# Optimization experiments

Hardware: AMD Instinct MI355X
Metric: run time of the kernel (lower is better)

## Reference

```python
import jax, jax.numpy as jnp
import numpy as np

B, T, U, D = 2, 512, 48, 512
H, K = 1024, 128  # hidden_channels, num_classes; fc1 in = 2*D = 1024


def setup_inputs() -> dict:
    key = jax.random.key(0)
    ks = jax.random.split(key, 9)
    s = 0.02
    return {
        "img_feature": jax.random.normal(ks[0], (B, T, D), jnp.float32),
        "label_feature": jax.random.normal(ks[1], (B, U, D), jnp.float32),
        "masks": jnp.ones((B, 1, T), jnp.float32),
        "W1": jax.random.normal(ks[2], (H, 2 * D), jnp.float32) * s,
        "b1": jnp.zeros((H,), jnp.float32),
        "W2": jax.random.normal(ks[3], (K, H), jnp.float32) * s,
        "b2": jnp.zeros((K,), jnp.float32),
        "conv_w": jax.random.normal(ks[4], (K, D), jnp.float32) * s,
        "conv_b": jnp.zeros((K,), jnp.float32),
    }


def reference(img_feature, label_feature, masks, W1, b1, W2, b2, conv_w, conv_b):
    # pointwise Conv1d over img features: (B,T,D) -> (B,K,T), masked
    img_seg_score = (jnp.einsum('btd,kd->bkt', img_feature, conv_w)
                     + conv_b[None, :, None]) * masks
    # fc1(cat(label, img)) == label @ Wl^T + img @ Wi^T + b1 (broadcast add),
    # avoiding the O(B*U*T*2D) repeat+cat intermediate.
    d = label_feature.shape[-1]
    Wl, Wi = W1[:, :d], W1[:, d:]
    lab = jnp.einsum('bud,hd->buh', label_feature, Wl)  # (B,U,H)
    img = jnp.einsum('btd,hd->bth', img_feature, Wi)    # (B,T,H)
    h = jnp.tanh(lab[:, :, None, :] + img[:, None, :, :] + b1)  # (B,U,T,H)
    joint = jnp.einsum('buth,kh->butk', h, W2) + b2
    joint_score = jax.nn.log_softmax(joint, axis=-1)
    return (img_seg_score, joint_score)
```

## Files before the change

kernel.cpp:

```cpp
#include <hip/hip_runtime.h>
#include <math.h>

#define BB 2
#define TT 512
#define UU 48
#define DD 512
#define HH 1024
#define KK 128

typedef _Float16 f16x8 __attribute__((ext_vector_type(8)));
typedef __fp16 fp16x2_t __attribute__((ext_vector_type(2)));
typedef float floatx4 __attribute__((ext_vector_type(4)));

__device__ __forceinline__ void g2l16(const _Float16* g, _Float16* l) {
    __builtin_amdgcn_global_load_lds(
        (const __attribute__((address_space(1))) unsigned int*)g,
        (__attribute__((address_space(3))) unsigned int*)l, 16, 0, 0);
}

__device__ __forceinline__ f16x8 tanh8(f16x8 x) {
    f16x8 o;
#pragma unroll
    for (int i = 0; i < 8; i += 2) {
        float s0 = (float)x[i];
        float s1 = (float)x[i + 1];
        float e0 = __expf(s0 + s0);
        float e1 = __expf(s1 + s1);
        float r0 = __builtin_amdgcn_rcpf(e0 + 1.0f);
        float r1 = __builtin_amdgcn_rcpf(e1 + 1.0f);
        fp16x2_t p = __builtin_amdgcn_cvt_pkrtz(fmaf(-2.0f, r0, 1.0f),
                                                fmaf(-2.0f, r1, 1.0f));
        o[i] = (_Float16)p[0];
        o[i + 1] = (_Float16)p[1];
    }
    return o;
}

__global__ __launch_bounds__(256) void mid_kernel4(
    const float* __restrict__ img, const float* __restrict__ labf,
    const float* __restrict__ W1, const float* __restrict__ W2,
    const float* __restrict__ conv_w,
    const float* __restrict__ b1, const float* __restrict__ conv_b,
    const float* __restrict__ masks,
    _Float16* __restrict__ imgHf, _Float16* __restrict__ labHf,
    _Float16* __restrict__ W2s, float* __restrict__ seg_out) {
    int bid = blockIdx.x, tid = threadIdx.x;
    if (bid >= 312) {
        int base = (bid - 312) * 256 + tid;
#pragma unroll
        for (int i = 0; i < 32; ++i) {
            int o = base + i * 4096;
            int hg = o >> 10, kk2 = (o >> 3) & 127, hl = o & 7;
            W2s[o] = (_Float16)W2[(size_t)kk2 * HH + hg * 8 + hl];
        }
        return;
    }
    __shared__ __align__(16) _Float16 a_s[32][72];
    __shared__ __align__(16) _Float16 w_s[8192];
    const float* Arow;
    const float* Wbase;
    int r0, n0b, wstride, region;
    if (bid < 256) {
        region = 0; Arow = img; Wbase = W1 + 512; wstride = 1024;
        r0 = (bid & 31) * 32; n0b = (bid >> 5) * 128;
    } else if (bid < 280) {
        region = 1; Arow = labf; Wbase = W1; wstride = 1024;
        int i = bid - 256; r0 = (i % 3) * 32; n0b = (i / 3) * 128;
    } else {
        region = 2; Arow = img; Wbase = conv_w; wstride = 512;
        r0 = (bid - 280) * 32; n0b = 0;
    }
    int lane = tid & 63, wv = tid >> 6;
    int m0 = (wv & 1) * 16, n0w = (wv >> 1) * 64;
    int q = lane >> 4, r = lane & 15;
    int arow = tid >> 3, acol = (tid & 7) * 8;
    int wn = tid >> 3, wk = tid & 7;
    const float* aptr = &Arow[(size_t)(r0 + arow) * DD + acol];
    floatx4 acc[4] = {};
    float4 pa0, pa1, pw[4][2];
    pa0 = *(const float4*)aptr;
    pa1 = *(const float4*)(aptr + 4);
#pragma unroll
    for (int i2 = 0; i2 < 4; ++i2) {
        const float* wp_ = &Wbase[(size_t)(n0b + i2 * 32 + wn) * wstride + wk * 8];
        pw[i2][0] = *(const float4*)wp_;
        pw[i2][1] = *(const float4*)(wp_ + 4);
    }
    for (int c = 0; c < 8; ++c) {
        {
            f16x8 av;
            av[0] = (_Float16)pa0.x; av[1] = (_Float16)pa0.y;
            av[2] = (_Float16)pa0.z; av[3] = (_Float16)pa0.w;
            av[4] = (_Float16)pa1.x; av[5] = (_Float16)pa1.y;
            av[6] = (_Float16)pa1.z; av[7] = (_Float16)pa1.w;
            *(f16x8*)&a_s[arow][acol] = av;
#pragma unroll
            for (int i2 = 0; i2 < 4; ++i2) {
                f16x8 wvv;
                wvv[0] = (_Float16)pw[i2][0].x; wvv[1] = (_Float16)pw[i2][0].y;
                wvv[2] = (_Float16)pw[i2][0].z; wvv[3] = (_Float16)pw[i2][0].w;
                wvv[4] = (_Float16)pw[i2][1].x; wvv[5] = (_Float16)pw[i2][1].y;
                wvv[6] = (_Float16)pw[i2][1].z; wvv[7] = (_Float16)pw[i2][1].w;
                *(f16x8*)&w_s[((size_t)wk * 128 + i2 * 32 + wn) * 8] = wvv;
            }
        }
        __syncthreads();
        if (c < 7) {
            int cb = (c + 1) * 64;
            pa0 = *(const float4*)(aptr + cb);
            pa1 = *(const float4*)(aptr + cb + 4);
#pragma unroll
            for (int i2 = 0; i2 < 4; ++i2) {
                const float* wp_ =
                    &Wbase[(size_t)(n0b + i2 * 32 + wn) * wstride + cb + wk * 8];
                pw[i2][0] = *(const float4*)wp_;
                pw[i2][1] = *(const float4*)(wp_ + 4);
            }
        }
#pragma unroll
        for (int kt = 0; kt < 2; ++kt) {
            f16x8 af = *(const f16x8*)&a_s[m0 + r][kt * 32 + q * 8];
#pragma unroll
            for (int nt = 0; nt < 4; ++nt) {
                f16x8 bfv = *(const f16x8*)
                    &w_s[((kt * 4 + q) * 128 + n0w + nt * 16 + r) * 8];
                acc[nt] = __builtin_amdgcn_mfma_f32_16x16x32_f16(
                    af, bfv, acc[nt], 0, 0, 0);
            }
        }
        __syncthreads();
    }
    if (region == 0) {
#pragma unroll
        for (int nt = 0; nt < 4; ++nt) {
            int n = n0b + n0w + nt * 16 + r;
#pragma unroll
            for (int rr = 0; rr < 4; ++rr)
                imgHf[(size_t)(r0 + m0 + 4 * q + rr) * HH + n] =
                    (_Float16)acc[nt][rr];
        }
    } else if (region == 1) {
#pragma unroll
        for (int nt = 0; nt < 4; ++nt) {
            int n = n0b + n0w + nt * 16 + r;
            float bv = b1[n];
#pragma unroll
            for (int rr = 0; rr < 4; ++rr)
                labHf[(size_t)(r0 + m0 + 4 * q + rr) * HH + n] =
                    (_Float16)(acc[nt][rr] + bv);
        }
    } else {
#pragma unroll
        for (int nt = 0; nt < 4; ++nt) {
            int k = n0w + nt * 16 + r;
            float bv = conv_b[k];
#pragma unroll
            for (int rr = 0; rr < 4; ++rr) {
                int row = r0 + m0 + 4 * q + rr;
                int b = row >> 9, t = row & 511;
                seg_out[((size_t)b * KK + k) * TT + t] =
                    (acc[nt][rr] + bv) * masks[row];
            }
        }
    }
}

__global__ __launch_bounds__(256) void joint_kernel8(
    const _Float16* __restrict__ imgHf,
    const _Float16* __restrict__ labHf,
    const _Float16* __restrict__ W2s,
    const float* __restrict__ b2,
    float* __restrict__ out) {
    __shared__ __align__(16) _Float16 w_s[2][8192];
    int tid = threadIdx.x, bid = blockIdx.x;
    int t0 = (bid & 7) * 64;
    int rest = bid >> 3;
    int u = rest % UU, b = rest / UU;
    int lane = tid & 63, wv = tid >> 6;
    int q = lane >> 4, r = lane & 15;
    const _Float16* imgrow = imgHf + ((size_t)b * TT + t0 + wv * 16 + r) * HH;
    const _Float16* labrow = labHf + (size_t)(b * UU + u) * HH;
    int c0 = q * 8, c1 = 32 + q * 8;
    int ws_off = tid * 8;
    floatx4 acc[8] = {};
#pragma unroll
    for (int i2 = 0; i2 < 4; ++i2)
        g2l16(&W2s[i2 * 2048 + ws_off], &w_s[0][i2 * 2048 + ws_off]);
    f16x8 ivA = *(const f16x8*)&imgrow[c0];
    f16x8 ivB = *(const f16x8*)&imgrow[c1];
    f16x8 lvA = *(const f16x8*)&labrow[c0];
    f16x8 lvB = *(const f16x8*)&labrow[c1];
    __syncthreads();
#pragma unroll 2
    for (int c = 0; c < 16; ++c) {
        int buf = c & 1;
        if (c < 15) {
            const _Float16* wsrc = W2s + (size_t)(c + 1) * 8192;
#pragma unroll
            for (int i2 = 0; i2 < 4; ++i2)
                g2l16(&wsrc[i2 * 2048 + ws_off],
                      &w_s[buf ^ 1][i2 * 2048 + ws_off]);
        }
        f16x8 a0 = tanh8(ivA + lvA);
        f16x8 a1 = tanh8(ivB + lvB);
        if (c < 15) {
            int cb = (c + 1) * 64;
            ivA = *(const f16x8*)&imgrow[cb + c0];
            ivB = *(const f16x8*)&imgrow[cb + c1];
            lvA = *(const f16x8*)&labrow[cb + c0];
            lvB = *(const f16x8*)&labrow[cb + c1];
        }
#pragma unroll
        for (int nt = 0; nt < 8; ++nt) {
            f16x8 bf0 = *(const f16x8*)&w_s[buf][((0 + q) * 128 + nt * 16 + r) * 8];
            acc[nt] = __builtin_amdgcn_mfma_f32_16x16x32_f16(
                a0, bf0, acc[nt], 0, 0, 0);
        }
#pragma unroll
        for (int nt = 0; nt < 8; ++nt) {
            f16x8 bf1 = *(const f16x8*)&w_s[buf][((4 + q) * 128 + nt * 16 + r) * 8];
            acc[nt] = __builtin_amdgcn_mfma_f32_16x16x32_f16(
                a1, bf1, acc[nt], 0, 0, 0);
        }
        __syncthreads();
    }
    float b2v[8];
#pragma unroll
    for (int nt = 0; nt < 8; ++nt) b2v[nt] = b2[nt * 16 + r];
    float* orow = out + (((size_t)b * UU + u) * TT + t0 + wv * 16) * KK;
#pragma unroll
    for (int rr = 0; rr < 4; ++rr) {
        float v[8];
        float mx = -INFINITY;
#pragma unroll
        for (int nt = 0; nt < 8; ++nt) {
            v[nt] = acc[nt][rr] + b2v[nt];
            mx = fmaxf(mx, v[nt]);
        }
        mx = fmaxf(mx, __shfl_xor(mx, 1, 16));
        mx = fmaxf(mx, __shfl_xor(mx, 2, 16));
        mx = fmaxf(mx, __shfl_xor(mx, 4, 16));
        mx = fmaxf(mx, __shfl_xor(mx, 8, 16));
        float s = 0.f;
#pragma unroll
        for (int nt = 0; nt < 8; ++nt) s += __expf(v[nt] - mx);
        s += __shfl_xor(s, 1, 16);
        s += __shfl_xor(s, 2, 16);
        s += __shfl_xor(s, 4, 16);
        s += __shfl_xor(s, 8, 16);
        float lse = mx + __logf(s);
        int row = 4 * q + rr;
#pragma unroll
        for (int nt = 0; nt < 8; ++nt)
            orow[(size_t)row * KK + nt * 16 + r] = v[nt] - lse;
    }
}

extern "C" void kernel_launch(void* const* d_in, const int* in_sizes, int n_in,
                              void* d_out, int out_size, void* d_ws, size_t ws_size,
                              hipStream_t stream) {
    const float* img    = (const float*)d_in[0];
    const float* labf   = (const float*)d_in[1];
    const float* masks  = (const float*)d_in[2];
    const float* W1     = (const float*)d_in[3];
    const float* b1     = (const float*)d_in[4];
    const float* W2     = (const float*)d_in[5];
    const float* b2     = (const float*)d_in[6];
    const float* conv_w = (const float*)d_in[7];
    const float* conv_b = (const float*)d_in[8];
    float* out = (float*)d_out;

    _Float16* base  = (_Float16*)d_ws;
    _Float16* imgHf = base;
    _Float16* labHf = imgHf + 1024 * 1024;
    _Float16* W2s   = labHf + 96 * 1024;

    mid_kernel4<<<328, 256, 0, stream>>>(img, labf, W1, W2, conv_w,
                                         b1, conv_b, masks,
                                         imgHf, labHf, W2s, out);
    joint_kernel8<<<768, 256, 0, stream>>>(imgHf, labHf, W2s, b2,
                                           out + (size_t)BB * KK * TT);
}
```

Baseline: 125.1 us.

## Switch joint kernel to 32x32x16 MFMA with two-wave blocks

Rewrites the joint GEMM to use 32x32x16 f16 MFMA tiles, with each wave covering 32 time rows and all 128 classes across four accumulators. Blocks shrink from 256 to 128 threads (launch bounds 128, 2), and the W2 LDS staging is redone to match. Larger MFMA tiles raise arithmetic intensity per LDS read and cut the number of instructions. The cost is more accumulator registers per thread (64 floats), fewer threads to spread the tanh work over, and a different softmax shuffle pattern that now spans 32 lanes.

```diff
diff --git a/kernel.cpp b/kernel.cpp
--- a/kernel.cpp
+++ b/kernel.cpp
@@ -11,6 +11,7 @@
 typedef _Float16 f16x8 __attribute__((ext_vector_type(8)));
 typedef __fp16 fp16x2_t __attribute__((ext_vector_type(2)));
 typedef float floatx4 __attribute__((ext_vector_type(4)));
+typedef float floatx16 __attribute__((ext_vector_type(16)));
 
 __device__ __forceinline__ void g2l16(const _Float16* g, _Float16* l) {
     __builtin_amdgcn_global_load_lds(
@@ -165,7 +166,7 @@
     }
 }
 
-__global__ __launch_bounds__(256) void joint_kernel8(
+__global__ __launch_bounds__(128, 2) void joint_kernel9(
     const _Float16* __restrict__ imgHf,
     const _Float16* __restrict__ labHf,
     const _Float16* __restrict__ W2s,
@@ -177,19 +178,21 @@
     int rest = bid >> 3;
     int u = rest % UU, b = rest / UU;
     int lane = tid & 63, wv = tid >> 6;
-    int q = lane >> 4, r = lane & 15;
-    const _Float16* imgrow = imgHf + ((size_t)b * TT + t0 + wv * 16 + r) * HH;
+    int lo = lane & 31, hi = lane >> 5;
+    const _Float16* imgrow = imgHf + ((size_t)b * TT + t0 + wv * 32 + lo) * HH;
     const _Float16* labrow = labHf + (size_t)(b * UU + u) * HH;
-    int c0 = q * 8, c1 = 32 + q * 8;
+    int kb = hi * 8;
     int ws_off = tid * 8;
-    floatx4 acc[8] = {};
-#pragma unroll
-    for (int i2 = 0; i2 < 4; ++i2)
-        g2l16(&W2s[i2 * 2048 + ws_off], &w_s[0][i2 * 2048 + ws_off]);
-    f16x8 ivA = *(const f16x8*)&imgrow[c0];
-    f16x8 ivB = *(const f16x8*)&imgrow[c1];
-    f16x8 lvA = *(const f16x8*)&labrow[c0];
-    f16x8 lvB = *(const f16x8*)&labrow[c1];
+    floatx16 acc[4] = {};
+#pragma unroll
+    for (int i2 = 0; i2 < 8; ++i2)
+        g2l16(&W2s[i2 * 1024 + ws_off], &w_s[0][i2 * 1024 + ws_off]);
+    f16x8 iv[4], lv[4];
+#pragma unroll
+    for (int s = 0; s < 4; ++s) {
+        iv[s] = *(const f16x8*)&imgrow[s * 16 + kb];
+        lv[s] = *(const f16x8*)&labrow[s * 16 + kb];
+    }
     __syncthreads();
 #pragma unroll 2
     for (int c = 0; c < 16; ++c) {
@@ -197,62 +200,64 @@
         if (c < 15) {
             const _Float16* wsrc = W2s + (size_t)(c + 1) * 8192;
 #pragma unroll
-            for (int i2 = 0; i2 < 4; ++i2)
-                g2l16(&wsrc[i2 * 2048 + ws_off],
-                      &w_s[buf ^ 1][i2 * 2048 + ws_off]);
-        }
-        f16x8 a0 = tanh8(ivA + lvA);
-        f16x8 a1 = tanh8(ivB + lvB);
+            for (int i2 = 0; i2 < 8; ++i2)
+                g2l16(&wsrc[i2 * 1024 + ws_off],
+                      &w_s[buf ^ 1][i2 * 1024 + ws_off]);
+        }
+        f16x8 a[4];
+#pragma unroll
+        for (int s = 0; s < 4; ++s) a[s] = tanh8(iv[s] + lv[s]);
         if (c < 15) {
             int cb = (c + 1) * 64;
-            ivA = *(const f16x8*)&imgrow[cb + c0];
-            ivB = *(const f16x8*)&imgrow[cb + c1];
-            lvA = *(const f16x8*)&labrow[cb + c0];
-            lvB = *(const f16x8*)&labrow[cb + c1];
-        }
-#pragma unroll
-        for (int nt = 0; nt < 8; ++nt) {
-            f16x8 bf0 = *(const f16x8*)&w_s[buf][((0 + q) * 128 + nt * 16 + r) * 8];
-            acc[nt] = __builtin_amdgcn_mfma_f32_16x16x32_f16(
-                a0, bf0, acc[nt], 0, 0, 0);
-        }
-#pragma unroll
-        for (int nt = 0; nt < 8; ++nt) {
-            f16x8 bf1 = *(const f16x8*)&w_s[buf][((4 + q) * 128 + nt * 16 + r) * 8];
-            acc[nt] = __builtin_amdgcn_mfma_f32_16x16x32_f16(
-                a1, bf1, acc[nt], 0, 0, 0);
+#pragma unroll
+            for (int s = 0; s < 4; ++s) {
+                iv[s] = *(const f16x8*)&imgrow[cb + s * 16 + kb];
+                lv[s] = *(const f16x8*)&labrow[cb + s * 16 + kb];
+            }
+        }
+#pragma unroll
+        for (int s = 0; s < 4; ++s) {
+#pragma unroll
+            for (int ct = 0; ct < 4; ++ct) {
+                f16x8 bf = *(const f16x8*)
+                    &w_s[buf][((s * 2 + hi) * 128 + ct * 32 + lo) * 8];
+                acc[ct] = __builtin_amdgcn_mfma_f32_32x32x16_f16(
+                    a[s], bf, acc[ct], 0, 0, 0);
+            }
         }
         __syncthreads();
     }
-    float b2v[8];
-#pragma unroll
-    for (int nt = 0; nt < 8; ++nt) b2v[nt] = b2[nt * 16 + r];
-    float* orow = out + (((size_t)b * UU + u) * TT + t0 + wv * 16) * KK;
-#pragma unroll
-    for (int rr = 0; rr < 4; ++rr) {
-        float v[8];
+    float b2v[4];
+#pragma unroll
+    for (int ct = 0; ct < 4; ++ct) b2v[ct] = b2[ct * 32 + lo];
+    float* obase = out + (((size_t)b * UU + u) * TT + t0 + wv * 32) * KK;
+#pragma unroll
+    for (int reg = 0; reg < 16; ++reg) {
+        int row = (reg & 3) + 8 * (reg >> 2) + 4 * hi;
+        float v[4];
         float mx = -INFINITY;
 #pragma unroll
-        for (int nt = 0; nt < 8; ++nt) {
-            v[nt] = acc[nt][rr] + b2v[nt];
-            mx = fmaxf(mx, v[nt]);
-        }
-        mx = fmaxf(mx, __shfl_xor(mx, 1, 16));
-        mx = fmaxf(mx, __shfl_xor(mx, 2, 16));
-        mx = fmaxf(mx, __shfl_xor(mx, 4, 16));
-        mx = fmaxf(mx, __shfl_xor(mx, 8, 16));
+        for (int ct = 0; ct < 4; ++ct) {
+            v[ct] = acc[ct][reg] + b2v[ct];
+            mx = fmaxf(mx, v[ct]);
+        }
+        mx = fmaxf(mx, __shfl_xor(mx, 1, 32));
+        mx = fmaxf(mx, __shfl_xor(mx, 2, 32));
+        mx = fmaxf(mx, __shfl_xor(mx, 4, 32));
+        mx = fmaxf(mx, __shfl_xor(mx, 8, 32));
+        mx = fmaxf(mx, __shfl_xor(mx, 16, 32));
         float s = 0.f;
 #pragma unroll
-        for (int nt = 0; nt < 8; ++nt) s += __expf(v[nt] - mx);
-        s += __shfl_xor(s, 1, 16);
-        s += __shfl_xor(s, 2, 16);
-        s += __shfl_xor(s, 4, 16);
-        s += __shfl_xor(s, 8, 16);
+        for (int ct = 0; ct < 4; ++ct) s += __expf(v[ct] - mx);
+        s += __shfl_xor(s, 1, 32);
+        s += __shfl_xor(s, 2, 32);
+        s += __shfl_xor(s, 4, 32);
+        s += __shfl_xor(s, 8, 32);
+        s += __shfl_xor(s, 16, 32);
         float lse = mx + __logf(s);
-        int row = 4 * q + rr;
-#pragma unroll
-        for (int nt = 0; nt < 8; ++nt)
-            orow[(size_t)row * KK + nt * 16 + r] = v[nt] - lse;
+#pragma unroll
+        for (int ct = 0; ct < 4; ++ct)
+            obase[(size_t)row * KK + ct * 32 + lo] = v[ct] - lse;
     }
 }
 
@@ -278,6 +283,6 @@
     mid_kernel4<<<328, 256, 0, stream>>>(img, labf, W1, W2, conv_w,
                                          b1, conv_b, masks,
                                          imgHf, labHf, W2s, out);
-    joint_kernel8<<<768, 256, 0, stream>>>(imgHf, labHf, W2s, b2,
+    joint_kernel9<<<768, 128, 0, stream>>>(imgHf, labHf, W2s, b2,
                                            out + (size_t)BB * KK * TT);
 }
```

New measurement: 133.9 us. 1.07x slower.
